# Performance work log

Measured on AMD Instinct MI355X. Metric: run time of the kernel, lower is better.

Reference implementation:

```python
import jax, jax.numpy as jnp
import numpy as np

N = 50000      # nodes
E = 800000     # edges
IN = 128       # in_channels
HID = 128      # hidden_channels
OUT = 2        # out_channels (edge classes)
HEADS = 8      # EGConv default num_heads
BASES = 4      # EGConv default num_bases
FH = HID // HEADS  # per-head feature dim = 16


def _egconv(x, Wb, Wc, bc, b, row, col, norm, n):
    """One EGConv layer (aggregators=['symnorm']), self-loops already in row/col/norm.
    Wb: [in, BASES*FH] basis projection (no bias).
    Wc: [in, HEADS*BASES], bc: combination weights linear.
    b : [HID] output bias.
    """
    bases = x @ Wb                                            # [n, BASES*FH]
    msg = bases[row] * norm[:, None]                          # gather + symnorm scale
    agg = jax.ops.segment_sum(msg, col, num_segments=n)       # scatter-add -> [n, BASES*FH]
    w = (x @ Wc + bc).reshape(n, HEADS, BASES)                # per-node combination weights
    out = jnp.einsum('nhb,nbf->nhf', w, agg.reshape(n, BASES, FH))
    return out.reshape(n, HEADS * FH) + b


def setup_inputs() -> dict:
    key = jax.random.key(0)
    ks = jax.random.split(key, 12)
    s = 0.05
    inp = {
        'x': jax.random.normal(ks[0], (N, IN), jnp.float32),
        'edge_index': jax.random.randint(ks[1], (2, E), 0, N, jnp.int64),
        # conv1
        'Wb1': jax.random.normal(ks[2], (IN, BASES * FH), jnp.float32) * s,
        'Wc1': jax.random.normal(ks[3], (IN, HEADS * BASES), jnp.float32) * s,
        'bc1': jnp.zeros((HEADS * BASES,), jnp.float32),
        'b1': jnp.zeros((HID,), jnp.float32),
        # conv2
        'Wb2': jax.random.normal(ks[4], (HID, BASES * FH), jnp.float32) * s,
        'Wc2': jax.random.normal(ks[5], (HID, HEADS * BASES), jnp.float32) * s,
        'bc2': jnp.zeros((HEADS * BASES,), jnp.float32),
        'b2': jnp.zeros((HID,), jnp.float32),
        # edge classifier
        'Wcls': jax.random.normal(ks[6], (2 * HID, OUT), jnp.float32) * s,
        'bcls': jnp.zeros((OUT,), jnp.float32),
    }
    return inp


def reference(x, edge_index, Wb1, Wc1, bc1, b1, Wb2, Wc2, bc2, b2, Wcls, bcls):
    n = x.shape[0]
    # add self loops (EGConv default add_self_loops=True) + gcn_norm symnorm weights
    sl = jnp.arange(n, dtype=edge_index.dtype)
    row = jnp.concatenate([edge_index[0], sl])
    col = jnp.concatenate([edge_index[1], sl])
    deg = jax.ops.segment_sum(jnp.ones(row.shape[0], x.dtype), col, num_segments=n)
    dis = jnp.where(deg > 0, deg, 1.0) ** -0.5
    dis = jnp.where(deg > 0, dis, 0.0)
    norm = dis[row] * dis[col]                                # symnorm edge weight

    h = jax.nn.relu(_egconv(x, Wb1, Wc1, bc1, b1, row, col, norm, n))
    h = _egconv(h, Wb2, Wc2, bc2, b2, row, col, norm, n)

    # edge classifier: gather endpoint embeddings of ORIGINAL edges, concat, linear
    e = jnp.concatenate([h[edge_index[0]], h[edge_index[1]]], axis=-1)  # [E, 2*HID]
    return e @ Wcls + bcls
```

## Files before the change

kernel.cpp:

```cpp
#include <hip/hip_runtime.h>
#include <hip/hip_fp16.h>

#define NN 50000
#define EE 800000
#define NB_E2 1563
#define NWIN 4
#define WIN 12500
#define EPB 1024
#define NCHUNK 782

__global__ void k_count(const int* __restrict__ ei, int* cnt, unsigned* __restrict__ pk) {
    int t = blockIdx.x * 256 + threadIdx.x;
    if (t < EE / 2) {
        int2 cc = *(const int2*)(ei + EE + 2 * t);
        unsigned r0 = (unsigned)atomicAdd(&cnt[cc.x], 1);
        unsigned r1 = (unsigned)atomicAdd(&cnt[cc.y], 1);
        *(uint2*)(pk + 2 * t) = make_uint2((unsigned)cc.x | (r0 << 16),
                                           (unsigned)cc.y | (r1 << 16));
    }
}

__global__ void k_scan1(const int* __restrict__ cnt, int* sloc, int* bsum,
                        float* dis, int n) {
    __shared__ int s[256];
    int tid = threadIdx.x;
    int i = blockIdx.x * 256 + tid;
    int v = (i < n) ? cnt[i] : 0;
    if (i < n) dis[i] = rsqrtf((float)v + 1.0f);
    s[tid] = v;
    __syncthreads();
    for (int off = 1; off < 256; off <<= 1) {
        int t2 = 0;
        if (tid >= off) t2 = s[tid - off];
        __syncthreads();
        if (tid >= off) s[tid] += t2;
        __syncthreads();
    }
    if (i < n) sloc[i] = s[tid] - v;
    if (tid == 255) bsum[blockIdx.x] = s[255];
}

__global__ void k_scan23(const int* __restrict__ sloc, const int* __restrict__ bsum,
                         const int* __restrict__ cnt, int2* sd, int* starts,
                         int n, int nb) {
    __shared__ int sb[256];
    int tid = threadIdx.x, b = blockIdx.x;
    int v = (tid < nb && tid < b) ? bsum[tid] : 0;
    sb[tid] = v;
    __syncthreads();
    for (int off = 128; off; off >>= 1) {
        if (tid < off) sb[tid] += sb[tid + off];
        __syncthreads();
    }
    int boff = sb[0];
    int i = b * 256 + tid;
    if (i < n) {
        int st = sloc[i] + boff;
        sd[i] = make_int2(st, cnt[i]);
        starts[i] = st;
    }
}

__global__ __launch_bounds__(256) void k_fill(
    const int* __restrict__ ei, const unsigned* __restrict__ pk,
    const int* __restrict__ starts, int* __restrict__ csr)
{
    int w = blockIdx.x & (NWIN - 1);
    int chunk = blockIdx.x >> 2;
    int base = chunk * EPB + threadIdx.x * 4;
    unsigned lo = w * WIN, hi = lo + WIN;
    if (base + 3 < EE) {
        int4 rr = *(const int4*)(ei + base);
        uint4 pp = *(const uint4*)(pk + base);
        unsigned c0 = pp.x & 0xffffu, c1 = pp.y & 0xffffu;
        unsigned c2 = pp.z & 0xffffu, c3 = pp.w & 0xffffu;
        if (c0 >= lo && c0 < hi) csr[starts[c0] + (pp.x >> 16)] = rr.x;
        if (c1 >= lo && c1 < hi) csr[starts[c1] + (pp.y >> 16)] = rr.y;
        if (c2 >= lo && c2 < hi) csr[starts[c2] + (pp.z >> 16)] = rr.z;
        if (c3 >= lo && c3 < hi) csr[starts[c3] + (pp.w >> 16)] = rr.w;
    } else {
        for (int e = 0; e < 4; e++) {
            int t = base + e;
            if (t < EE) {
                unsigned pv = pk[t];
                unsigned c = pv & 0xffffu;
                if (c >= lo && c < hi) csr[starts[c] + (pv >> 16)] = ei[t];
            }
        }
    }
}

__global__ __launch_bounds__(256) void k_gemm(
    const float* __restrict__ x, const float* __restrict__ Wb,
    const float* __restrict__ Wc, const float* __restrict__ bc,
    const float* __restrict__ dis,
    __half* __restrict__ bsh, float* __restrict__ wcomb, int n)
{
    __shared__ float xt[32 * 257];
    int tid = threadIdx.x;
    int grp = blockIdx.y;
    int row0 = blockIdx.x * 256;
    int row = row0 + tid;
    bool valid = row < n;

    const float* W = (grp < 2) ? (Wb + grp * 32) : Wc;
    const int ldw = (grp < 2) ? 64 : 32;

    float acc[32];
#pragma unroll
    for (int c = 0; c < 32; c++) acc[c] = 0.f;

    for (int s = 0; s < 4; s++) {
        int base_k = s * 32;
        float4 v[8];
#pragma unroll
        for (int i = 0; i < 8; i++) {
            int idx = i * 256 + tid;
            int r = idx >> 3;
            int k4 = idx & 7;
            int gr = row0 + r;
            v[i] = (gr < n) ? *(const float4*)(x + (size_t)gr * 128 + base_k + k4 * 4)
                            : make_float4(0.f, 0.f, 0.f, 0.f);
        }
        __syncthreads();
#pragma unroll
        for (int i = 0; i < 8; i++) {
            int idx = i * 256 + tid;
            int r = idx >> 3;
            int k4 = idx & 7;
            xt[(k4 * 4 + 0) * 257 + r] = v[i].x;
            xt[(k4 * 4 + 1) * 257 + r] = v[i].y;
            xt[(k4 * 4 + 2) * 257 + r] = v[i].z;
            xt[(k4 * 4 + 3) * 257 + r] = v[i].w;
        }
        __syncthreads();

        const float* Ws = W + base_k * ldw;
#pragma unroll 8
        for (int k = 0; k < 32; k++) {
            float xs = xt[k * 257 + tid];
            const float* wk = Ws + k * ldw;
#pragma unroll
            for (int c = 0; c < 32; c++) acc[c] = fmaf(xs, wk[c], acc[c]);
        }
    }

    if (!valid) return;
    if (grp < 2) {
        float d = dis[row];
        __half2 hh[16];
#pragma unroll
        for (int c = 0; c < 16; c++)
            hh[c] = __floats2half2_rn(acc[2 * c] * d, acc[2 * c + 1] * d);
        uint4* bo = (uint4*)(bsh + (size_t)row * 64 + grp * 32);
        const uint4* src = (const uint4*)hh;
#pragma unroll
        for (int c = 0; c < 4; c++) bo[c] = src[c];
    } else {
        float4* wo = (float4*)(wcomb + (size_t)row * 32);
#pragma unroll
        for (int c = 0; c < 8; c++)
            wo[c] = make_float4(acc[4*c] + bc[4*c], acc[4*c+1] + bc[4*c+1],
                                acc[4*c+2] + bc[4*c+2], acc[4*c+3] + bc[4*c+3]);
    }
}

template<int LAYER2>
__global__ __launch_bounds__(256) void k_agg(
    const int* __restrict__ csr, const int2* __restrict__ sd,
    const __half* __restrict__ bsh, const float* __restrict__ dis,
    const float* __restrict__ wcomb, const float* __restrict__ bias,
    float* __restrict__ h,
    const float* __restrict__ Wcls, const float* __restrict__ bcls,
    float* __restrict__ p, int n)
{
    int wid = (blockIdx.x * 256 + threadIdx.x) >> 6;
    int lane = threadIdx.x & 63;
    if (wid >= n) return;
    int2 s2 = sd[wid];
    int start = s2.x, deg = s2.y;
    int g = lane >> 4, q = lane & 15;

    const uint2* bsp = (const uint2*)bsh;
    float4 acc4 = make_float4(0.f, 0.f, 0.f, 0.f);
    if (g == 0) {
        uint2 v = bsp[(size_t)wid * 16 + q];
        float2 lo = __half22float2(*(const __half2*)&v.x);
        float2 hi = __half22float2(*(const __half2*)&v.y);
        acc4 = make_float4(lo.x, lo.y, hi.x, hi.y);
    }

    int j = 0;
    int ia = 0, ib = 0;
    if (8 <= deg) { ia = csr[start + g]; ib = csr[start + 4 + g]; }
    while (j + 8 <= deg) {
        int jn = j + 8;
        int na = 0, nb = 0;
        if (jn + 8 <= deg) { na = csr[start + jn + g]; nb = csr[start + jn + 4 + g]; }
        uint2 v0 = bsp[(size_t)ia * 16 + q];
        uint2 v1 = bsp[(size_t)ib * 16 + q];
        float2 l0 = __half22float2(*(const __half2*)&v0.x);
        float2 h0 = __half22float2(*(const __half2*)&v0.y);
        float2 l1 = __half22float2(*(const __half2*)&v1.x);
        float2 h1 = __half22float2(*(const __half2*)&v1.y);
        acc4.x += l0.x + l1.x;
        acc4.y += l0.y + l1.y;
        acc4.z += h0.x + h1.x;
        acc4.w += h0.y + h1.y;
        ia = na; ib = nb; j = jn;
    }
    int last = start + deg - 1;
    for (; j < deg; j += 4) {
        int idx = start + j + g;
        int r = csr[min(idx, last)];
        uint2 v = bsp[(size_t)r * 16 + q];
        float2 lo = __half22float2(*(const __half2*)&v.x);
        float2 hi = __half22float2(*(const __half2*)&v.y);
        float m = (j + g < deg) ? 1.f : 0.f;
        acc4.x = fmaf(lo.x, m, acc4.x);
        acc4.y = fmaf(lo.y, m, acc4.y);
        acc4.z = fmaf(hi.x, m, acc4.z);
        acc4.w = fmaf(hi.y, m, acc4.w);
    }

    acc4.x += __shfl_xor(acc4.x, 16, 64);
    acc4.y += __shfl_xor(acc4.y, 16, 64);
    acc4.z += __shfl_xor(acc4.z, 16, 64);
    acc4.w += __shfl_xor(acc4.w, 16, 64);
    acc4.x += __shfl_xor(acc4.x, 32, 64);
    acc4.y += __shfl_xor(acc4.y, 32, 64);
    acc4.z += __shfl_xor(acc4.z, 32, 64);
    acc4.w += __shfl_xor(acc4.w, 32, 64);

    float d = dis[wid];
    acc4.x *= d; acc4.y *= d; acc4.z *= d; acc4.w *= d;

    int src = lane >> 2;
    float t0 = __shfl(acc4.x, src, 64);
    float t1 = __shfl(acc4.y, src, 64);
    float t2 = __shfl(acc4.z, src, 64);
    float t3 = __shfl(acc4.w, src, 64);
    int c = lane & 3;
    float acc = (c == 0) ? t0 : (c == 1) ? t1 : (c == 2) ? t2 : t3;

    int fh = lane & 15;
    float a0 = __shfl(acc, fh, 64);
    float a1 = __shfl(acc, 16 + fh, 64);
    float a2 = __shfl(acc, 32 + fh, 64);
    float a3 = __shfl(acc, 48 + fh, 64);
    const float* wn = wcomb + (size_t)wid * 32;
    int hd = lane >> 4;
    float s1 = bias[lane];
    float s2v = bias[64 + lane];
    s1 = fmaf(wn[hd * 4 + 0], a0, s1);
    s1 = fmaf(wn[hd * 4 + 1], a1, s1);
    s1 = fmaf(wn[hd * 4 + 2], a2, s1);
    s1 = fmaf(wn[hd * 4 + 3], a3, s1);
    s2v = fmaf(wn[(4 + hd) * 4 + 0], a0, s2v);
    s2v = fmaf(wn[(4 + hd) * 4 + 1], a1, s2v);
    s2v = fmaf(wn[(4 + hd) * 4 + 2], a2, s2v);
    s2v = fmaf(wn[(4 + hd) * 4 + 3], a3, s2v);

    if (!LAYER2) {
        s1 = fmaxf(s1, 0.f);
        s2v = fmaxf(s2v, 0.f);
        h[(size_t)wid * 128 + lane] = s1;
        h[(size_t)wid * 128 + 64 + lane] = s2v;
    } else {
        float r0 = s1 * Wcls[lane * 2 + 0] + s2v * Wcls[(64 + lane) * 2 + 0];
        float r1 = s1 * Wcls[lane * 2 + 1] + s2v * Wcls[(64 + lane) * 2 + 1];
        float r2 = s1 * Wcls[(128 + lane) * 2 + 0] + s2v * Wcls[(192 + lane) * 2 + 0];
        float r3 = s1 * Wcls[(128 + lane) * 2 + 1] + s2v * Wcls[(192 + lane) * 2 + 1];
#pragma unroll
        for (int off = 32; off; off >>= 1) {
            r0 += __shfl_xor(r0, off, 64);
            r1 += __shfl_xor(r1, off, 64);
            r2 += __shfl_xor(r2, off, 64);
            r3 += __shfl_xor(r3, off, 64);
        }
        if (lane == 0) {
            p[wid * 4 + 0] = r0 + bcls[0];
            p[wid * 4 + 1] = r1 + bcls[1];
            p[wid * 4 + 2] = r2;
            p[wid * 4 + 3] = r3;
        }
    }
}

__global__ void k_edge(const int* __restrict__ ei, const float* __restrict__ p,
                       float* __restrict__ out)
{
    int t = blockIdx.x * blockDim.x + threadIdx.x;
    if (t >= EE / 2) return;
    int2 rr = *(const int2*)(ei + 2 * t);
    int2 cc = *(const int2*)(ei + EE + 2 * t);
    float2 pt0 = *(const float2*)(p + rr.x * 4);
    float2 pt1 = *(const float2*)(p + rr.y * 4);
    float2 pb0 = *(const float2*)(p + cc.x * 4 + 2);
    float2 pb1 = *(const float2*)(p + cc.y * 4 + 2);
    float4 o;
    o.x = pt0.x + pb0.x;
    o.y = pt0.y + pb0.y;
    o.z = pt1.x + pb1.x;
    o.w = pt1.y + pb1.y;
    *(float4*)(out + (size_t)t * 4) = o;
}

extern "C" void kernel_launch(void* const* d_in, const int* in_sizes, int n_in,
                              void* d_out, int out_size, void* d_ws, size_t ws_size,
                              hipStream_t stream) {
    const float* x    = (const float*)d_in[0];
    const int*   ei   = (const int*)d_in[1];
    const float* Wb1  = (const float*)d_in[2];
    const float* Wc1  = (const float*)d_in[3];
    const float* bc1  = (const float*)d_in[4];
    const float* b1   = (const float*)d_in[5];
    const float* Wb2  = (const float*)d_in[6];
    const float* Wc2  = (const float*)d_in[7];
    const float* bc2  = (const float*)d_in[8];
    const float* b2   = (const float*)d_in[9];
    const float* Wcls = (const float*)d_in[10];
    const float* bcls = (const float*)d_in[11];
    float* out = (float*)d_out;

    char* ws = (char*)d_ws;
    size_t off = 0;
    auto alloc = [&](size_t bytes) {
        void* pp = ws + off;
        off += (bytes + 15) & ~(size_t)15;
        return pp;
    };

    float*    dis    = (float*)alloc(50048 * 4);
    __half*   bsh    = (__half*)alloc((size_t)NN * 64 * 2);
    float*    wcomb  = (float*)alloc((size_t)NN * 32 * 4);
    float*    h      = (float*)alloc((size_t)NN * 128 * 4);
    float*    p      = (float*)alloc((size_t)NN * 4 * 4);
    int*      cnt    = (int*)alloc(50048 * 4);
    int*      sloc   = (int*)alloc(50048 * 4);
    int*      starts = (int*)alloc(50048 * 4);
    int*      bsum   = (int*)alloc(256 * 4);
    int2*     sd     = (int2*)alloc((size_t)50048 * 8);
    int*      csr    = (int*)alloc((size_t)EE * 4);
    unsigned* pk     = (unsigned*)alloc((size_t)EE * 4);

    const int B = 256;
    int gN   = (NN + B - 1) / B;
    int gN64 = (NN * 64) / B;
    dim3 gG(gN, 3);

    hipMemsetAsync(cnt, 0, NN * sizeof(int), stream);
    k_count<<<NB_E2, B, 0, stream>>>(ei, cnt, pk);
    k_scan1<<<gN, B, 0, stream>>>(cnt, sloc, bsum, dis, NN);
    k_scan23<<<gN, B, 0, stream>>>(sloc, bsum, cnt, sd, starts, NN, gN);
    k_fill<<<NCHUNK * NWIN, B, 0, stream>>>(ei, pk, starts, csr);

    k_gemm<<<gG, B, 0, stream>>>(x, Wb1, Wc1, bc1, dis, bsh, wcomb, NN);
    k_agg<0><<<gN64, B, 0, stream>>>(csr, sd, bsh, dis, wcomb, b1, h,
                                     Wcls, bcls, p, NN);

    k_gemm<<<gG, B, 0, stream>>>(h, Wb2, Wc2, bc2, dis, bsh, wcomb, NN);
    k_agg<1><<<gN64, B, 0, stream>>>(csr, sd, bsh, dis, wcomb, b2, h,
                                     Wcls, bcls, p, NN);

    k_edge<<<NB_E2, B, 0, stream>>>(ei, p, out);
}
```

Measured before the change: 275.6 us.

## Merge scan kernels, fuse CSR fill with layer-1 GEMM, widen count loads

The two-pass scan becomes a single kernel in which each block recomputes its prefix offset by summing all earlier counts directly. The CSR fill and the first-layer GEMM now run as one launch with block-index dispatch, so the two independent jobs can overlap. The edge count kernel handles four edges per thread with int4 loads. This removes two launches and the intermediate sloc/bsum buffers, at the cost of redundant prefix summation (later scan blocks reread up to all 50k counts) and a 33KB shared allocation reserved even by fill blocks, which may lower their occupancy.

```diff
diff --git a/kernel.cpp b/kernel.cpp
--- a/kernel.cpp
+++ b/kernel.cpp
@@ -4,102 +4,85 @@
 #define NN 50000
 #define EE 800000
 #define NB_E2 1563
+#define NB_CNT 782
 #define NWIN 4
 #define WIN 12500
 #define EPB 1024
 #define NCHUNK 782
+#define NFILL (NCHUNK * NWIN)
+#define NGEMM 588
 
 __global__ void k_count(const int* __restrict__ ei, int* cnt, unsigned* __restrict__ pk) {
     int t = blockIdx.x * 256 + threadIdx.x;
-    if (t < EE / 2) {
-        int2 cc = *(const int2*)(ei + EE + 2 * t);
+    int base = t * 4;
+    if (base + 3 < EE) {
+        int4 cc = *(const int4*)(ei + EE + base);
         unsigned r0 = (unsigned)atomicAdd(&cnt[cc.x], 1);
         unsigned r1 = (unsigned)atomicAdd(&cnt[cc.y], 1);
-        *(uint2*)(pk + 2 * t) = make_uint2((unsigned)cc.x | (r0 << 16),
-                                           (unsigned)cc.y | (r1 << 16));
-    }
-}
-
-__global__ void k_scan1(const int* __restrict__ cnt, int* sloc, int* bsum,
-                        float* dis, int n) {
+        unsigned r2 = (unsigned)atomicAdd(&cnt[cc.z], 1);
+        unsigned r3 = (unsigned)atomicAdd(&cnt[cc.w], 1);
+        *(uint4*)(pk + base) = make_uint4((unsigned)cc.x | (r0 << 16),
+                                          (unsigned)cc.y | (r1 << 16),
+                                          (unsigned)cc.z | (r2 << 16),
+                                          (unsigned)cc.w | (r3 << 16));
+    } else {
+        for (int e = 0; e < 4; e++) {
+            int tt = base + e;
+            if (tt < EE) {
+                int c = ei[EE + tt];
+                unsigned r = (unsigned)atomicAdd(&cnt[c], 1);
+                pk[tt] = (unsigned)c | (r << 16);
+            }
+        }
+    }
+}
+
+__global__ void k_scan(const int* __restrict__ cnt, float* __restrict__ dis,
+                       int2* __restrict__ sd, int* __restrict__ starts, int n) {
     __shared__ int s[256];
-    int tid = threadIdx.x;
-    int i = blockIdx.x * 256 + tid;
+    int tid = threadIdx.x, b = blockIdx.x;
+    int i = b * 256 + tid;
     int v = (i < n) ? cnt[i] : 0;
     if (i < n) dis[i] = rsqrtf((float)v + 1.0f);
     s[tid] = v;
     __syncthreads();
     for (int off = 1; off < 256; off <<= 1) {
-        int t2 = 0;
-        if (tid >= off) t2 = s[tid - off];
+        int t2 = (tid >= off) ? s[tid - off] : 0;
         __syncthreads();
         if (tid >= off) s[tid] += t2;
         __syncthreads();
     }
-    if (i < n) sloc[i] = s[tid] - v;
-    if (tid == 255) bsum[blockIdx.x] = s[255];
-}
-
-__global__ void k_scan23(const int* __restrict__ sloc, const int* __restrict__ bsum,
-                         const int* __restrict__ cnt, int2* sd, int* starts,
-                         int n, int nb) {
-    __shared__ int sb[256];
-    int tid = threadIdx.x, b = blockIdx.x;
-    int v = (tid < nb && tid < b) ? bsum[tid] : 0;
-    sb[tid] = v;
+    int loc = s[tid] - v;
+    int lim = b * 256;
+    int pre = 0;
+    for (int j = tid * 4; j < lim; j += 1024) {
+        int4 c4 = *(const int4*)(cnt + j);
+        pre += c4.x + c4.y + c4.z + c4.w;
+    }
+    __syncthreads();
+    s[tid] = pre;
     __syncthreads();
     for (int off = 128; off; off >>= 1) {
-        if (tid < off) sb[tid] += sb[tid + off];
-        __syncthreads();
-    }
-    int boff = sb[0];
-    int i = b * 256 + tid;
+        if (tid < off) s[tid] += s[tid + off];
+        __syncthreads();
+    }
+    int boff = s[0];
     if (i < n) {
-        int st = sloc[i] + boff;
-        sd[i] = make_int2(st, cnt[i]);
+        int st = loc + boff;
+        sd[i] = make_int2(st, v);
         starts[i] = st;
     }
 }
 
-__global__ __launch_bounds__(256) void k_fill(
-    const int* __restrict__ ei, const unsigned* __restrict__ pk,
-    const int* __restrict__ starts, int* __restrict__ csr)
-{
-    int w = blockIdx.x & (NWIN - 1);
-    int chunk = blockIdx.x >> 2;
-    int base = chunk * EPB + threadIdx.x * 4;
-    unsigned lo = w * WIN, hi = lo + WIN;
-    if (base + 3 < EE) {
-        int4 rr = *(const int4*)(ei + base);
-        uint4 pp = *(const uint4*)(pk + base);
-        unsigned c0 = pp.x & 0xffffu, c1 = pp.y & 0xffffu;
-        unsigned c2 = pp.z & 0xffffu, c3 = pp.w & 0xffffu;
-        if (c0 >= lo && c0 < hi) csr[starts[c0] + (pp.x >> 16)] = rr.x;
-        if (c1 >= lo && c1 < hi) csr[starts[c1] + (pp.y >> 16)] = rr.y;
-        if (c2 >= lo && c2 < hi) csr[starts[c2] + (pp.z >> 16)] = rr.z;
-        if (c3 >= lo && c3 < hi) csr[starts[c3] + (pp.w >> 16)] = rr.w;
-    } else {
-        for (int e = 0; e < 4; e++) {
-            int t = base + e;
-            if (t < EE) {
-                unsigned pv = pk[t];
-                unsigned c = pv & 0xffffu;
-                if (c >= lo && c < hi) csr[starts[c] + (pv >> 16)] = ei[t];
-            }
-        }
-    }
-}
-
-__global__ __launch_bounds__(256) void k_gemm(
+__device__ __forceinline__ void gemm_body(
+    float* xt, int bx, int grp,
     const float* __restrict__ x, const float* __restrict__ Wb,
     const float* __restrict__ Wc, const float* __restrict__ bc,
     const float* __restrict__ dis,
     __half* __restrict__ bsh, float* __restrict__ wcomb, int n)
 {
-    __shared__ float xt[32 * 257];
     int tid = threadIdx.x;
-    int grp = blockIdx.y;
-    int row0 = blockIdx.x * 256;
+    int row0 = bx * 256;
     int row = row0 + tid;
     bool valid = row < n;
 
@@ -163,6 +146,55 @@
             wo[c] = make_float4(acc[4*c] + bc[4*c], acc[4*c+1] + bc[4*c+1],
                                 acc[4*c+2] + bc[4*c+2], acc[4*c+3] + bc[4*c+3]);
     }
+}
+
+__global__ __launch_bounds__(256) void k_fillgemm(
+    const int* __restrict__ ei, const unsigned* __restrict__ pk,
+    const int* __restrict__ starts, int* __restrict__ csr,
+    const float* __restrict__ x, const float* __restrict__ Wb,
+    const float* __restrict__ Wc, const float* __restrict__ bc,
+    const float* __restrict__ dis,
+    __half* __restrict__ bsh, float* __restrict__ wcomb, int n)
+{
+    __shared__ float xt[32 * 257];
+    if (blockIdx.x < NFILL) {
+        int w = blockIdx.x & (NWIN - 1);
+        int chunk = blockIdx.x >> 2;
+        int base = chunk * EPB + threadIdx.x * 4;
+        unsigned lo = w * WIN, hi = lo + WIN;
+        if (base + 3 < EE) {
+            int4 rr = *(const int4*)(ei + base);
+            uint4 pp = *(const uint4*)(pk + base);
+            unsigned c0 = pp.x & 0xffffu, c1 = pp.y & 0xffffu;
+            unsigned c2 = pp.z & 0xffffu, c3 = pp.w & 0xffffu;
+            if (c0 >= lo && c0 < hi) csr[starts[c0] + (pp.x >> 16)] = rr.x;
+            if (c1 >= lo && c1 < hi) csr[starts[c1] + (pp.y >> 16)] = rr.y;
+            if (c2 >= lo && c2 < hi) csr[starts[c2] + (pp.z >> 16)] = rr.z;
+            if (c3 >= lo && c3 < hi) csr[starts[c3] + (pp.w >> 16)] = rr.w;
+        } else {
+            for (int e = 0; e < 4; e++) {
+                int t = base + e;
+                if (t < EE) {
+                    unsigned pv = pk[t];
+                    unsigned c = pv & 0xffffu;
+                    if (c >= lo && c < hi) csr[starts[c] + (pv >> 16)] = ei[t];
+                }
+            }
+        }
+        return;
+    }
+    int b2 = blockIdx.x - NFILL;
+    gemm_body(xt, b2 / 3, b2 % 3, x, Wb, Wc, bc, dis, bsh, wcomb, n);
+}
+
+__global__ __launch_bounds__(256) void k_gemm(
+    const float* __restrict__ x, const float* __restrict__ Wb,
+    const float* __restrict__ Wc, const float* __restrict__ bc,
+    const float* __restrict__ dis,
+    __half* __restrict__ bsh, float* __restrict__ wcomb, int n)
+{
+    __shared__ float xt[32 * 257];
+    gemm_body(xt, blockIdx.x, blockIdx.y, x, Wb, Wc, bc, dis, bsh, wcomb, n);
 }
 
 template<int LAYER2>
@@ -337,9 +369,7 @@
     float*    h      = (float*)alloc((size_t)NN * 128 * 4);
     float*    p      = (float*)alloc((size_t)NN * 4 * 4);
     int*      cnt    = (int*)alloc(50048 * 4);
-    int*      sloc   = (int*)alloc(50048 * 4);
     int*      starts = (int*)alloc(50048 * 4);
-    int*      bsum   = (int*)alloc(256 * 4);
     int2*     sd     = (int2*)alloc((size_t)50048 * 8);
     int*      csr    = (int*)alloc((size_t)EE * 4);
     unsigned* pk     = (unsigned*)alloc((size_t)EE * 4);
@@ -350,12 +380,11 @@
     dim3 gG(gN, 3);
 
     hipMemsetAsync(cnt, 0, NN * sizeof(int), stream);
-    k_count<<<NB_E2, B, 0, stream>>>(ei, cnt, pk);
-    k_scan1<<<gN, B, 0, stream>>>(cnt, sloc, bsum, dis, NN);
-    k_scan23<<<gN, B, 0, stream>>>(sloc, bsum, cnt, sd, starts, NN, gN);
-    k_fill<<<NCHUNK * NWIN, B, 0, stream>>>(ei, pk, starts, csr);
-
-    k_gemm<<<gG, B, 0, stream>>>(x, Wb1, Wc1, bc1, dis, bsh, wcomb, NN);
+    k_count<<<NB_CNT, B, 0, stream>>>(ei, cnt, pk);
+    k_scan<<<gN, B, 0, stream>>>(cnt, dis, sd, starts, NN);
+    k_fillgemm<<<NFILL + NGEMM, B, 0, stream>>>(ei, pk, starts, csr,
+                                                x, Wb1, Wc1, bc1, dis, bsh, wcomb, NN);
+
     k_agg<0><<<gN64, B, 0, stream>>>(csr, sd, bsh, dis, wcomb, b1, h,
                                      Wcls, bcls, p, NN);
 
```

After: 281.2 us. 1.02x slower.
